# Kernel tuning notes

Hardware: AMD Instinct MI355X
Metric: run time of the kernel (lower is better)

## Reference

```python
import jax, jax.numpy as jnp
import numpy as np

D_MODEL = 1024
HEADDIM = 64
EXPAND = 2
D_STATE = 128
D_CONV = 4
NGROUPS = 1
D_INNER = EXPAND * D_MODEL            # 2048
NHEADS = D_INNER // HEADDIM           # 32
CONV_DIM = D_INNER + 2 * NGROUPS * D_STATE
D_IN_PROJ = 2 * D_INNER + 2 * NGROUPS * D_STATE + NHEADS
BATCH = 2
SEQLEN = 1024
EPS = 1e-5


def silu(v):
    return v * jax.nn.sigmoid(v)


def setup_inputs() -> dict:
    key = jax.random.key(0)
    ks = jax.random.split(key, 8)
    s = 0.02
    return {
        "x": jax.random.normal(ks[0], (BATCH, SEQLEN, D_MODEL), jnp.float32),
        "in_proj_w": jax.random.normal(ks[1], (D_IN_PROJ, D_MODEL), jnp.float32) * s,
        "conv_w": jax.random.normal(ks[2], (CONV_DIM, D_CONV), jnp.float32) * 0.2,
        "conv_b": jax.random.normal(ks[3], (CONV_DIM,), jnp.float32) * 0.02,
        "dt_bias": jax.random.normal(ks[4], (NHEADS,), jnp.float32) * 0.1,
        "A_log": jax.random.normal(ks[5], (NHEADS,), jnp.float32) * 0.5,
        "D": jax.random.normal(ks[6], (NHEADS,), jnp.float32) * 0.5,
        "norm_w": jnp.ones((D_INNER,), jnp.float32),
        "out_proj_w": jax.random.normal(ks[7], (D_MODEL, D_INNER), jnp.float32) * s,
    }


def _mamba2(x, in_proj_w, conv_w, conv_b, dt_bias, A_log, D, norm_w, out_proj_w):
    b, l, _ = x.shape
    # input projection -> z | xBC | dt
    zxbcdt = x @ in_proj_w.T                                  # [b,l,d_in_proj]
    z, xBC, dt = jnp.split(zxbcdt, [D_INNER, D_INNER + CONV_DIM], axis=-1)
    dt = jax.nn.softplus(dt + dt_bias)                        # [b,l,nh]
    # causal depthwise conv over time, then SiLU
    rhs = conv_w.T[:, None, :]                                # [d_conv, 1, conv_dim]
    xBC = jax.lax.conv_general_dilated(
        xBC, rhs, window_strides=(1,), padding=[(D_CONV - 1, 0)],
        dimension_numbers=("NWC", "WIO", "NWC"), feature_group_count=CONV_DIM)
    xBC = silu(xBC + conv_b)
    xs, Bm, Cm = jnp.split(xBC, [D_INNER, D_INNER + D_STATE], axis=-1)
    xs = xs.reshape(b, l, NHEADS, HEADDIM)                    # [b,l,h,p]
    A = -jnp.exp(A_log)                                       # [nh], negative
    dA = jnp.exp(dt * A)                                      # [b,l,nh] in (0,1)
    # selective scan: h_t = dA_t * h_{t-1} + dt_t * x_t (outer) B_t; y_t = h_t C_t
    def step(h, inp):
        dA_t, x_t, B_t, dt_t, C_t = inp                       # [b,h],[b,h,p],[b,n],[b,h],[b,n]
        h = h * dA_t[:, :, None, None] + jnp.einsum("bh,bhp,bn->bhpn", dt_t, x_t, B_t)
        y = jnp.einsum("bhpn,bn->bhp", h, C_t)
        return h, y

    h0 = jnp.zeros((b, NHEADS, HEADDIM, D_STATE), x.dtype)
    xs_t = xs.transpose(1, 0, 2, 3)
    _, ys = jax.lax.scan(step, h0, (dA.transpose(1, 0, 2), xs_t,
                                    Bm.transpose(1, 0, 2), dt.transpose(1, 0, 2),
                                    Cm.transpose(1, 0, 2)))
    y = ys.transpose(1, 0, 2, 3) + D[None, None, :, None] * xs  # skip term
    y = y.reshape(b, l, D_INNER)
    # gated RMSNorm (norm_before_gate=False): rmsnorm(y * silu(z)) * w
    y = y * silu(z)
    y = y * jax.lax.rsqrt(jnp.mean(y * y, axis=-1, keepdims=True) + EPS) * norm_w
    return y @ out_proj_w.T


def reference(x, in_proj_w, conv_w, conv_b, dt_bias, A_log, D, norm_w, out_proj_w):
    return x + _mamba2(x, in_proj_w, conv_w, conv_b, dt_bias, A_log, D, norm_w, out_proj_w)
```

## Files before the change

### kernel.cpp

```cpp
#include <hip/hip_runtime.h>
#include <hip/hip_bf16.h>
#include <math.h>

#define NHEADS   32
#define CONV_DIM 2304
#define D_INNER  2048
#define SEQLEN   1024
#define NROWS    2048
#define ZX_STR   4352
#define D_MODEL  1024
#define Q        64
#define NCHUNK   16
#define XT_STR   72

typedef __attribute__((ext_vector_type(8))) short bhalf8;
typedef __attribute__((ext_vector_type(8))) short short8;
typedef __attribute__((ext_vector_type(4))) short short4v;
typedef __attribute__((ext_vector_type(4))) float f32x4;

__device__ __forceinline__ float bf2f(__hip_bfloat16 v){ return __bfloat162float(v); }
__device__ __forceinline__ short f2bs(float f){ __hip_bfloat16 h = __float2bfloat16(f); return *(short*)&h; }
__device__ __forceinline__ float s2f(short s){ __hip_bfloat16 h = *(__hip_bfloat16*)&s; return __bfloat162float(h); }
__device__ __forceinline__ float rdin(const void* p, size_t i, int isf){
    return isf ? ((const float*)p)[i] : __bfloat162float(((const __hip_bfloat16*)p)[i]);
}

__global__ __launch_bounds__(256)
void detect_dtype(const unsigned short* __restrict__ p, int* __restrict__ flag)
{
    int cnt = 0;
    for (int i = threadIdx.x; i < 4096; i += 256) {
        unsigned short u = p[2 * i];
        int e = (u >> 7) & 0xFF;
        cnt += (e >= 90 && e <= 141) ? 1 : 0;
    }
#pragma unroll
    for (int m = 1; m < 64; m <<= 1) cnt += __shfl_xor(cnt, m);
    __shared__ int red[4];
    if ((threadIdx.x & 63) == 0) red[threadIdx.x >> 6] = cnt;
    __syncthreads();
    if (threadIdx.x == 0) *flag = ((red[0]+red[1]+red[2]+red[3]) < 2048) ? 1 : 0;
}

#define XN8 262144
#define WN8 561152
#define ON8 262144
__global__ __launch_bounds__(256)
void to_bf16_all(const void* __restrict__ xs, const void* __restrict__ ws,
                 const void* __restrict__ os,
                 __hip_bfloat16* __restrict__ xd, __hip_bfloat16* __restrict__ wd,
                 __hip_bfloat16* __restrict__ od, const int* __restrict__ flagp)
{
    const int isf = *flagp;
    int i = blockIdx.x * 256 + threadIdx.x;
    const void* src; __hip_bfloat16* dst; int j;
    if (i < XN8)            { src = xs; dst = xd; j = i; }
    else if (i < XN8 + WN8) { src = ws; dst = wd; j = i - XN8; }
    else                    { src = os; dst = od; j = i - XN8 - WN8; }
    if (isf) {
        const float4* s = (const float4*)src;
        float4 a = s[2 * j], b = s[2 * j + 1];
        short8 r;
        r[0]=f2bs(a.x); r[1]=f2bs(a.y); r[2]=f2bs(a.z); r[3]=f2bs(a.w);
        r[4]=f2bs(b.x); r[5]=f2bs(b.y); r[6]=f2bs(b.z); r[7]=f2bs(b.w);
        ((short8*)dst)[j] = r;
    } else {
        ((float4*)dst)[j] = ((const float4*)src)[j];
    }
}

template<int MODE, int MT, int NT, int WROWS, int WCOLS>
__global__ __launch_bounds__(256)
void gemm_bt(const __hip_bfloat16* __restrict__ A,
             const __hip_bfloat16* __restrict__ W,
             __hip_bfloat16* __restrict__ Cb,
             const void* __restrict__ xraw,
             void* __restrict__ outv,
             const int* __restrict__ flagp,
             int K, int N)
{
    constexpr int FM = MT / WROWS / 16;
    constexpr int FN = NT / WCOLS / 16;
    constexpr int AI = MT / 32;
    constexpr int BI = NT / 32;
    __shared__ short As[MT * 64];
    __shared__ short Bs[NT * 64];
    const int m0 = blockIdx.y * MT;
    const int n0 = blockIdx.x * NT;
    const int wave = threadIdx.x >> 6;
    const int lane = threadIdx.x & 63;
    const int lr8 = lane >> 3, lc8 = lane & 7;
    const int lr  = lane & 15, lq  = lane >> 4;
    const int wm = (wave / WCOLS) * (MT / WROWS);
    const int wn = (wave % WCOLS) * (NT / WCOLS);
    const int swl = lr & 7;

    f32x4 acc[FM][FN];
#pragma unroll
    for (int i = 0; i < FM; ++i)
#pragma unroll
        for (int j = 0; j < FN; ++j) acc[i][j] = (f32x4){0.f,0.f,0.f,0.f};

    for (int k0 = 0; k0 < K; k0 += 64) {
#pragma unroll
        for (int i = 0; i < AI; ++i) {
            const int rt = (wave * AI + i) * 8;
            const __hip_bfloat16* gp = A + (size_t)(m0 + rt + lr8) * K + k0 + ((lc8 ^ lr8) << 3);
            __builtin_amdgcn_global_load_lds(
                (const __attribute__((address_space(1))) void*)gp,
                (__attribute__((address_space(3))) void*)&As[rt * 64], 16, 0, 0);
        }
#pragma unroll
        for (int i = 0; i < BI; ++i) {
            const int rt = (wave * BI + i) * 8;
            const __hip_bfloat16* gp = W + (size_t)(n0 + rt + lr8) * K + k0 + ((lc8 ^ lr8) << 3);
            __builtin_amdgcn_global_load_lds(
                (const __attribute__((address_space(1))) void*)gp,
                (__attribute__((address_space(3))) void*)&Bs[rt * 64], 16, 0, 0);
        }
        __syncthreads();
#pragma unroll
        for (int kk = 0; kk < 64; kk += 32) {
            const int sw = (((kk >> 3) + lq) ^ swl) << 3;
            bhalf8 af[FM], bfv[FN];
#pragma unroll
            for (int t = 0; t < FM; ++t)
                af[t]  = *(const bhalf8*)&As[(wm + t * 16 + lr) * 64 + sw];
#pragma unroll
            for (int t = 0; t < FN; ++t)
                bfv[t] = *(const bhalf8*)&Bs[(wn + t * 16 + lr) * 64 + sw];
#pragma unroll
            for (int ti = 0; ti < FM; ++ti)
#pragma unroll
                for (int tj = 0; tj < FN; ++tj)
                    acc[ti][tj] = __builtin_amdgcn_mfma_f32_16x16x32_bf16(
                        af[ti], bfv[tj], acc[ti][tj], 0, 0, 0);
        }
        __syncthreads();
    }

    const int isf = (MODE == 1) ? *flagp : 0;
#pragma unroll
    for (int ti = 0; ti < FM; ++ti)
#pragma unroll
        for (int tj = 0; tj < FN; ++tj)
#pragma unroll
            for (int r = 0; r < 4; ++r) {
                int m = m0 + wm + ti * 16 + lq * 4 + r;
                int n = n0 + wn + tj * 16 + lr;
                size_t idx = (size_t)m * N + n;
                float v = acc[ti][tj][r];
                if (MODE == 0) {
                    Cb[idx] = __float2bfloat16(v);
                } else {
                    v += rdin(xraw, idx, isf);
                    if (isf) ((float*)outv)[idx] = v;
                    else     ((__hip_bfloat16*)outv)[idx] = __float2bfloat16(v);
                }
            }
}

__global__ __launch_bounds__(256)
void dt_kernel(const void* __restrict__ xraw, const void* __restrict__ wraw,
               const void* __restrict__ dt_bias,
               const int* __restrict__ flagp,
               float* __restrict__ dtp)
{
    const int isf = *flagp;
    const int r0 = blockIdx.x * 8;
    __shared__ float xs[8][D_MODEL];
    for (int idx = threadIdx.x; idx < 8 * D_MODEL; idx += 256)
        ((float*)xs)[idx] = rdin(xraw, (size_t)r0 * D_MODEL + idx, isf);
    __syncthreads();
    const int h = threadIdx.x >> 3;
    const int t = threadIdx.x & 7;
    const size_t wbase = (size_t)(4352 + h) * D_MODEL;
    float s[8];
#pragma unroll
    for (int r = 0; r < 8; ++r) s[r] = 0.f;
    for (int k = t; k < D_MODEL; k += 8) {
        float wv = rdin(wraw, wbase + k, isf);
#pragma unroll
        for (int r = 0; r < 8; ++r) s[r] = fmaf(xs[r][k], wv, s[r]);
    }
#pragma unroll
    for (int r = 0; r < 8; ++r) {
        s[r] += __shfl_xor(s[r], 1);
        s[r] += __shfl_xor(s[r], 2);
        s[r] += __shfl_xor(s[r], 4);
    }
    if (t == 0) {
        float bias = rdin(dt_bias, h, isf);
#pragma unroll
        for (int r = 0; r < 8; ++r) {
            float raw = s[r] + bias;
            dtp[(size_t)(r0 + r) * NHEADS + h] = raw > 20.f ? raw : log1pf(expf(raw));
        }
    }
}

__global__ __launch_bounds__(256)
void conv_silu(const __hip_bfloat16* __restrict__ zxb,
               const void* __restrict__ conv_w, const void* __restrict__ conv_b,
               const int* __restrict__ flagp,
               __hip_bfloat16* __restrict__ xs_bf,
               __hip_bfloat16* __restrict__ B_bf,
               __hip_bfloat16* __restrict__ C_bf)
{
    __shared__ short buf[11 * CONV_DIM];
    const int isf = *flagp;
    const int r0 = blockIdx.x * 8;
    const int bstart = r0 & ~(SEQLEN - 1);
    for (int idx = threadIdx.x; idx < 11 * (CONV_DIM / 8); idx += 256) {
        int ii = idx / (CONV_DIM / 8);
        int seg = idx % (CONV_DIM / 8);
        int g = r0 - 3 + ii;
        bhalf8 v;
        if (g >= bstart) {
            v = *(const bhalf8*)&zxb[(size_t)g * ZX_STR + 2048 + seg * 8];
        } else {
#pragma unroll
            for (int j = 0; j < 8; ++j) v[j] = 0;
        }
        *(bhalf8*)&buf[ii * CONV_DIM + seg * 8] = v;
    }
    __syncthreads();

#pragma unroll
    for (int j = 0; j < CONV_DIM / 256; ++j) {
        const int c = threadIdx.x + j * 256;
        float w0 = rdin(conv_w, (size_t)c * 4 + 0, isf);
        float w1 = rdin(conv_w, (size_t)c * 4 + 1, isf);
        float w2 = rdin(conv_w, (size_t)c * 4 + 2, isf);
        float w3 = rdin(conv_w, (size_t)c * 4 + 3, isf);
        float bias = rdin(conv_b, c, isf);
#pragma unroll
        for (int r = 0; r < 8; ++r) {
            float acc = bias;
            acc = fmaf(s2f(buf[(r + 0) * CONV_DIM + c]), w0, acc);
            acc = fmaf(s2f(buf[(r + 1) * CONV_DIM + c]), w1, acc);
            acc = fmaf(s2f(buf[(r + 2) * CONV_DIM + c]), w2, acc);
            acc = fmaf(s2f(buf[(r + 3) * CONV_DIM + c]), w3, acc);
            float v = acc / (1.f + expf(-acc));
            __hip_bfloat16 bv = __float2bfloat16(v);
            int row = r0 + r;
            if (c < 2048)       xs_bf[(size_t)row * 2048 + c] = bv;
            else if (c < 2176)  B_bf[(size_t)row * 128 + (c - 2048)] = bv;
            else                C_bf[(size_t)row * 128 + (c - 2176)] = bv;
        }
    }
}

__global__ __launch_bounds__(256)
void chunk_kernel(const __hip_bfloat16* __restrict__ xs_bf,
                  const __hip_bfloat16* __restrict__ B_bf,
                  const __hip_bfloat16* __restrict__ C_bf,
                  const float* __restrict__ dtp, const void* __restrict__ Alog,
                  const int* __restrict__ flagp,
                  float* __restrict__ cumg, float* __restrict__ decayg,
                  __hip_bfloat16* __restrict__ M_bf, float* __restrict__ S)
{
    __shared__ float cumS[Q], uS[Q], dtS[Q];
    __shared__ short Xt[64 * XT_STR];
    __shared__ short Bt[128 * XT_STR];
    const int bhc = blockIdx.x;
    const int c = bhc & 15, h = (bhc >> 4) & 31, b = bhc >> 9;
    const int row0 = b * SEQLEN + c * Q;
    const int isf = *flagp;

    if (threadIdx.x < 64) {
        const int t = threadIdx.x;
        const float An = -expf(rdin(Alog, h, isf));
        const float dt = dtp[(size_t)(row0 + t) * NHEADS + h];
        float cum = dt * An;
#pragma unroll
        for (int ofs = 1; ofs < 64; ofs <<= 1) {
            float v = __shfl_up(cum, ofs);
            if (t >= ofs) cum += v;
        }
        float tot = __shfl(cum, 63);
        cumS[t] = cum; dtS[t] = dt;
        uS[t] = expf(tot - cum) * dt;
        cumg[(size_t)bhc * Q + t] = cum;
        if (t == 63) decayg[bhc] = expf(tot);
    }
    __syncthreads();

#pragma unroll
    for (int i = 0; i < 2; ++i) {
        int seg = threadIdx.x + i * 256;
        int t = seg >> 3, p8 = (seg & 7) * 8;
        float ut = uS[t];
        bhalf8 v = *(const bhalf8*)&xs_bf[(size_t)(row0 + t) * 2048 + h * 64 + p8];
#pragma unroll
        for (int j = 0; j < 8; ++j)
            Xt[(p8 + j) * XT_STR + t] = f2bs(s2f(v[j]) * ut);
    }
#pragma unroll
    for (int i = 0; i < 4; ++i) {
        int seg = threadIdx.x + i * 256;
        int t = seg >> 4, n8 = (seg & 15) * 8;
        bhalf8 v = *(const bhalf8*)&B_bf[(size_t)(row0 + t) * 128 + n8];
#pragma unroll
        for (int j = 0; j < 8; ++j)
            Bt[(n8 + j) * XT_STR + t] = v[j];
    }

    const int wave = threadIdx.x >> 6, lane = threadIdx.x & 63;
    const int lr = lane & 15, lq = lane >> 4;

    {
        const int t0 = wave * 16;
        f32x4 acc[4];
#pragma unroll
        for (int j = 0; j < 4; ++j) acc[j] = (f32x4){0.f,0.f,0.f,0.f};
#pragma unroll
        for (int kk = 0; kk < 128; kk += 32) {
            bhalf8 af = *(const bhalf8*)&C_bf[(size_t)(row0 + t0 + lr) * 128 + kk + lq * 8];
#pragma unroll
            for (int j = 0; j < 4; ++j) {
                bhalf8 bf = *(const bhalf8*)&B_bf[(size_t)(row0 + j * 16 + lr) * 128 + kk + lq * 8];
                acc[j] = __builtin_amdgcn_mfma_f32_16x16x32_bf16(af, bf, acc[j], 0, 0, 0);
            }
        }
#pragma unroll
        for (int j = 0; j < 4; ++j)
#pragma unroll
            for (int r = 0; r < 4; ++r) {
                int t = t0 + lq * 4 + r;
                int s = j * 16 + lr;
                float m = (s <= t) ? acc[j][r] * expf(cumS[t] - cumS[s]) * dtS[s] : 0.f;
                M_bf[(size_t)bhc * 4096 + t * 64 + s] = __float2bfloat16(m);
            }
    }
    __syncthreads();

    {
        const int p0 = wave * 16;
        f32x4 acc[8];
#pragma unroll
        for (int j = 0; j < 8; ++j) acc[j] = (f32x4){0.f,0.f,0.f,0.f};
#pragma unroll
        for (int kk = 0; kk < 64; kk += 32) {
            bhalf8 af = *(const bhalf8*)&Xt[(p0 + lr) * XT_STR + kk + lq * 8];
#pragma unroll
            for (int j = 0; j < 8; ++j) {
                bhalf8 bf = *(const bhalf8*)&Bt[(j * 16 + lr) * XT_STR + kk + lq * 8];
                acc[j] = __builtin_amdgcn_mfma_f32_16x16x32_bf16(af, bf, acc[j], 0, 0, 0);
            }
        }
#pragma unroll
        for (int j = 0; j < 8; ++j)
#pragma unroll
            for (int r = 0; r < 4; ++r) {
                int p = p0 + lq * 4 + r;
                int n = j * 16 + lr;
                S[(size_t)bhc * 8192 + p * 128 + n] = acc[j][r];
            }
    }
}

__global__ __launch_bounds__(256)
void rec_kernel(const float* __restrict__ S, const float* __restrict__ decayg,
                __hip_bfloat16* __restrict__ hst)
{
    const int bh = blockIdx.x >> 3;
    const int sl = blockIdx.x & 7;
    const int off = sl * 1024 + threadIdx.x * 4;
    float h0 = 0.f, h1 = 0.f, h2 = 0.f, h3 = 0.f;
    for (int c = 0; c < NCHUNK; ++c) {
        size_t base = ((size_t)bh * NCHUNK + c) * 8192 + off;
        short4v hb;
        hb[0] = f2bs(h0); hb[1] = f2bs(h1); hb[2] = f2bs(h2); hb[3] = f2bs(h3);
        *(short4v*)&hst[base] = hb;
        float4 s = *(const float4*)&S[base];
        float d = decayg[bh * NCHUNK + c];
        h0 = fmaf(h0, d, s.x); h1 = fmaf(h1, d, s.y);
        h2 = fmaf(h2, d, s.z); h3 = fmaf(h3, d, s.w);
    }
}

__global__ __launch_bounds__(256)
void y_kernel(const __hip_bfloat16* __restrict__ M_bf,
              const __hip_bfloat16* __restrict__ xs_bf,
              const __hip_bfloat16* __restrict__ C_bf,
              const __hip_bfloat16* __restrict__ hst,
              const float* __restrict__ cumg,
              const void* __restrict__ Draw, const int* __restrict__ flagp,
              float* __restrict__ yws)
{
    __shared__ short Xt[64 * XT_STR];
    const int bhc = blockIdx.x;
    const int c = bhc & 15, h = (bhc >> 4) & 31, b = bhc >> 9;
    const int row0 = b * SEQLEN + c * Q;
    const int isf = *flagp;
    const float Dh = rdin(Draw, h, isf);

#pragma unroll
    for (int i = 0; i < 2; ++i) {
        int seg = threadIdx.x + i * 256;
        int t = seg >> 3, p8 = (seg & 7) * 8;
        bhalf8 v = *(const bhalf8*)&xs_bf[(size_t)(row0 + t) * 2048 + h * 64 + p8];
#pragma unroll
        for (int j = 0; j < 8; ++j)
            Xt[(p8 + j) * XT_STR + t] = v[j];
    }
    __syncthreads();

    const int wave = threadIdx.x >> 6, lane = threadIdx.x & 63;
    const int lr = lane & 15, lq = lane >> 4;
    const int t0 = wave * 16;
    f32x4 acc1[4], acc2[4];
#pragma unroll
    for (int j = 0; j < 4; ++j) { acc1[j] = (f32x4){0.f,0.f,0.f,0.f}; acc2[j] = acc1[j]; }

#pragma unroll
    for (int kk = 0; kk < 64; kk += 32) {
        bhalf8 af = *(const bhalf8*)&M_bf[(size_t)bhc * 4096 + (t0 + lr) * 64 + kk + lq * 8];
#pragma unroll
        for (int j = 0; j < 4; ++j) {
            bhalf8 bf = *(const bhalf8*)&Xt[(j * 16 + lr) * XT_STR + kk + lq * 8];
            acc1[j] = __builtin_amdgcn_mfma_f32_16x16x32_bf16(af, bf, acc1[j], 0, 0, 0);
        }
    }
#pragma unroll
    for (int kk = 0; kk < 128; kk += 32) {
        bhalf8 af = *(const bhalf8*)&C_bf[(size_t)(row0 + t0 + lr) * 128 + kk + lq * 8];
#pragma unroll
        for (int j = 0; j < 4; ++j) {
            bhalf8 bf = *(const bhalf8*)&hst[(size_t)bhc * 8192 + (j * 16 + lr) * 128 + kk + lq * 8];
            acc2[j] = __builtin_amdgcn_mfma_f32_16x16x32_bf16(af, bf, acc2[j], 0, 0, 0);
        }
    }
    float ex[4];
#pragma unroll
    for (int r = 0; r < 4; ++r) ex[r] = expf(cumg[(size_t)bhc * Q + t0 + lq * 4 + r]);
#pragma unroll
    for (int j = 0; j < 4; ++j)
#pragma unroll
        for (int r = 0; r < 4; ++r) {
            int t = t0 + lq * 4 + r;
            int p = j * 16 + lr;
            float xv = s2f(Xt[p * XT_STR + t]);
            float y = acc1[j][r] + ex[r] * acc2[j][r] + Dh * xv;
            yws[(size_t)(row0 + t) * D_INNER + h * 64 + p] = y;
        }
}

__global__ __launch_bounds__(256)
void gate_norm(const float* __restrict__ yws,
               const __hip_bfloat16* __restrict__ zxb,
               const void* __restrict__ norm_w,
               const int* __restrict__ flagp,
               __hip_bfloat16* __restrict__ yg)
{
    const int isf = *flagp;
    const int row = blockIdx.x;
    const float* y = yws + (size_t)row * D_INNER;
    const __hip_bfloat16* z = zxb + (size_t)row * ZX_STR;
    float v[8]; float ss = 0.f;
#pragma unroll
    for (int it = 0; it < 8; ++it) {
        int c = it * 256 + threadIdx.x;
        float zz = bf2f(z[c]);
        float vv = y[c] * (zz / (1.f + expf(-zz)));
        v[it] = vv;
        ss += vv * vv;
    }
#pragma unroll
    for (int m = 1; m < 64; m <<= 1) ss += __shfl_xor(ss, m);
    __shared__ float red[4];
    if ((threadIdx.x & 63) == 0) red[threadIdx.x >> 6] = ss;
    __syncthreads();
    float tot = red[0] + red[1] + red[2] + red[3];
    float scale = rsqrtf(tot / (float)D_INNER + 1e-5f);
#pragma unroll
    for (int it = 0; it < 8; ++it) {
        int c = it * 256 + threadIdx.x;
        yg[(size_t)row * D_INNER + c] =
            __float2bfloat16(v[it] * scale * rdin(norm_w, c, isf));
    }
}

extern "C" void kernel_launch(void* const* d_in, const int* in_sizes, int n_in,
                              void* d_out, int out_size, void* d_ws, size_t ws_size,
                              hipStream_t stream)
{
    const void* x_raw    = d_in[0];
    const void* inw_raw  = d_in[1];
    const void* convw    = d_in[2];
    const void* convb    = d_in[3];
    const void* dtb      = d_in[4];
    const void* Alog     = d_in[5];
    const void* Dsk      = d_in[6];
    const void* normw    = d_in[7];
    const void* outw_raw = d_in[8];

    char* ws = (char*)d_ws;
    size_t off = 0;
    int* flag = (int*)(ws + off);                      off += 256;
    __hip_bfloat16* xb    = (__hip_bfloat16*)(ws+off); off += (size_t)NROWS * D_MODEL * 2;
    __hip_bfloat16* inwb  = (__hip_bfloat16*)(ws+off); off += (size_t)4384 * D_MODEL * 2;
    __hip_bfloat16* outwb = (__hip_bfloat16*)(ws+off); off += (size_t)D_MODEL * D_INNER * 2;
    __hip_bfloat16* zxb   = (__hip_bfloat16*)(ws+off); off += (size_t)NROWS * ZX_STR * 2;
    __hip_bfloat16* xs_bf = (__hip_bfloat16*)(ws+off); off += (size_t)NROWS * 2048 * 2;
    __hip_bfloat16* B_bf  = (__hip_bfloat16*)(ws+off); off += (size_t)NROWS * 128 * 2;
    __hip_bfloat16* C_bf  = (__hip_bfloat16*)(ws+off); off += (size_t)NROWS * 128 * 2;
    float* dtp   = (float*)(ws+off);                   off += (size_t)NROWS * NHEADS * 4;
    float* cumg  = (float*)(ws+off);                   off += (size_t)1024 * Q * 4;
    float* decayg= (float*)(ws+off);                   off += (size_t)1024 * 4;
    __hip_bfloat16* M_bf  = (__hip_bfloat16*)(ws+off); off += (size_t)1024 * 4096 * 2;
    __hip_bfloat16* hst   = (__hip_bfloat16*)(ws+off); off += (size_t)1024 * 8192 * 2;
    float* S = (float*)(ws+off);                       off += (size_t)1024 * 8192 * 4;
    float* yws = S;
    __hip_bfloat16* yg = (__hip_bfloat16*)(S + (size_t)NROWS * D_INNER);

    detect_dtype<<<1, 256, 0, stream>>>((const unsigned short*)x_raw, flag);
    to_bf16_all<<<(XN8+WN8+ON8)/256, 256, 0, stream>>>(x_raw, inw_raw, outw_raw,
                                                       xb, inwb, outwb, flag);
    gemm_bt<0,64,128,1,4><<<dim3(34, 32), 256, 0, stream>>>(
        xb, inwb, zxb, nullptr, nullptr, flag, D_MODEL, ZX_STR);
    dt_kernel<<<256, 256, 0, stream>>>(x_raw, inw_raw, dtb, flag, dtp);
    conv_silu<<<256, 256, 0, stream>>>(zxb, convw, convb, flag, xs_bf, B_bf, C_bf);
    chunk_kernel<<<1024, 256, 0, stream>>>(xs_bf, B_bf, C_bf, dtp, Alog, flag,
                                           cumg, decayg, M_bf, S);
    rec_kernel<<<512, 256, 0, stream>>>(S, decayg, hst);
    y_kernel<<<1024, 256, 0, stream>>>(M_bf, xs_bf, C_bf, hst, cumg, Dsk, flag, yws);
    gate_norm<<<NROWS, 256, 0, stream>>>(yws, zxb, normw, flag, yg);
    gemm_bt<1,64,64,2,2><<<dim3(16, 32), 256, 0, stream>>>(
        yg, outwb, nullptr, x_raw, d_out, flag, D_INNER, D_MODEL);
}
```

Baseline: 256.7 us.

## Fuse conv/dt kernels, gate into y_kernel, and store chunk states in bf16

Merges the dt projection and causal conv kernels into one launch split by block index, and vectorizes the conv to 8-channel bf16 loads and stores. Moves the SiLU gating and the sum of squares into y_kernel, using atomics into a per-row accumulator that detect_dtype zeroes, so the final pass only applies the RMS scale. It also stores chunk states and the gated output in bf16 instead of fp32 to halve that traffic. The cost is extra rounding in the state recurrence and the pre-norm values, plus atomic contention on row sums.

Result: faster. 248.8 us (-3.1%).

```diff
diff --git a/kernel.cpp b/kernel.cpp
--- a/kernel.cpp
+++ b/kernel.cpp
@@ -26,8 +26,10 @@
 }
 
 __global__ __launch_bounds__(256)
-void detect_dtype(const unsigned short* __restrict__ p, int* __restrict__ flag)
-{
+void detect_dtype(const unsigned short* __restrict__ p, int* __restrict__ flag,
+                  float* __restrict__ rowsum)
+{
+    for (int i = threadIdx.x; i < NROWS; i += 256) rowsum[i] = 0.f;
     int cnt = 0;
     for (int i = threadIdx.x; i < 4096; i += 256) {
         unsigned short u = p[2 * i];
@@ -161,92 +163,106 @@
 }
 
 __global__ __launch_bounds__(256)
-void dt_kernel(const void* __restrict__ xraw, const void* __restrict__ wraw,
-               const void* __restrict__ dt_bias,
-               const int* __restrict__ flagp,
-               float* __restrict__ dtp)
-{
+void convdt(const __hip_bfloat16* __restrict__ zxb,
+            const void* __restrict__ conv_w, const void* __restrict__ conv_b,
+            const void* __restrict__ xraw, const void* __restrict__ wraw,
+            const void* __restrict__ dt_bias,
+            const int* __restrict__ flagp,
+            __hip_bfloat16* __restrict__ xs_bf,
+            __hip_bfloat16* __restrict__ B_bf,
+            __hip_bfloat16* __restrict__ C_bf,
+            float* __restrict__ dtp)
+{
+    __shared__ short smem[11 * CONV_DIM];
     const int isf = *flagp;
-    const int r0 = blockIdx.x * 8;
-    __shared__ float xs[8][D_MODEL];
-    for (int idx = threadIdx.x; idx < 8 * D_MODEL; idx += 256)
-        ((float*)xs)[idx] = rdin(xraw, (size_t)r0 * D_MODEL + idx, isf);
-    __syncthreads();
-    const int h = threadIdx.x >> 3;
-    const int t = threadIdx.x & 7;
-    const size_t wbase = (size_t)(4352 + h) * D_MODEL;
-    float s[8];
-#pragma unroll
-    for (int r = 0; r < 8; ++r) s[r] = 0.f;
-    for (int k = t; k < D_MODEL; k += 8) {
-        float wv = rdin(wraw, wbase + k, isf);
-#pragma unroll
-        for (int r = 0; r < 8; ++r) s[r] = fmaf(xs[r][k], wv, s[r]);
-    }
-#pragma unroll
-    for (int r = 0; r < 8; ++r) {
-        s[r] += __shfl_xor(s[r], 1);
-        s[r] += __shfl_xor(s[r], 2);
-        s[r] += __shfl_xor(s[r], 4);
-    }
-    if (t == 0) {
-        float bias = rdin(dt_bias, h, isf);
+
+    if (blockIdx.x < 256) {
+        const int r0 = blockIdx.x * 8;
+        const int bstart = r0 & ~(SEQLEN - 1);
+        for (int idx = threadIdx.x; idx < 11 * (CONV_DIM / 8); idx += 256) {
+            int ii = idx / (CONV_DIM / 8);
+            int seg = idx % (CONV_DIM / 8);
+            int g = r0 - 3 + ii;
+            bhalf8 v;
+            if (g >= bstart) {
+                v = *(const bhalf8*)&zxb[(size_t)g * ZX_STR + 2048 + seg * 8];
+            } else {
+#pragma unroll
+                for (int j = 0; j < 8; ++j) v[j] = 0;
+            }
+            *(bhalf8*)&smem[ii * CONV_DIM + seg * 8] = v;
+        }
+        __syncthreads();
+
+#pragma unroll
+        for (int sIt = 0; sIt < 2; ++sIt) {
+            const int seg = threadIdx.x + sIt * 256;
+            if (seg >= CONV_DIM / 8) break;
+            const int c0 = seg * 8;
+            float w0[8], w1[8], w2[8], w3[8], bias[8];
+#pragma unroll
+            for (int j = 0; j < 8; ++j) {
+                bias[j] = rdin(conv_b, c0 + j, isf);
+                w0[j] = rdin(conv_w, (size_t)(c0 + j) * 4 + 0, isf);
+                w1[j] = rdin(conv_w, (size_t)(c0 + j) * 4 + 1, isf);
+                w2[j] = rdin(conv_w, (size_t)(c0 + j) * 4 + 2, isf);
+                w3[j] = rdin(conv_w, (size_t)(c0 + j) * 4 + 3, isf);
+            }
+#pragma unroll
+            for (int r = 0; r < 8; ++r) {
+                bhalf8 i0 = *(const bhalf8*)&smem[(r + 0) * CONV_DIM + c0];
+                bhalf8 i1 = *(const bhalf8*)&smem[(r + 1) * CONV_DIM + c0];
+                bhalf8 i2 = *(const bhalf8*)&smem[(r + 2) * CONV_DIM + c0];
+                bhalf8 i3 = *(const bhalf8*)&smem[(r + 3) * CONV_DIM + c0];
+                bhalf8 out;
+#pragma unroll
+                for (int j = 0; j < 8; ++j) {
+                    float acc = bias[j];
+                    acc = fmaf(s2f(i0[j]), w0[j], acc);
+                    acc = fmaf(s2f(i1[j]), w1[j], acc);
+                    acc = fmaf(s2f(i2[j]), w2[j], acc);
+                    acc = fmaf(s2f(i3[j]), w3[j], acc);
+                    out[j] = f2bs(acc / (1.f + expf(-acc)));
+                }
+                const int row = r0 + r;
+                if (c0 < 2048)
+                    *(bhalf8*)&xs_bf[(size_t)row * 2048 + c0] = out;
+                else if (c0 < 2176)
+                    *(bhalf8*)&B_bf[(size_t)row * 128 + (c0 - 2048)] = out;
+                else
+                    *(bhalf8*)&C_bf[(size_t)row * 128 + (c0 - 2176)] = out;
+            }
+        }
+    } else {
+        float* xsh = (float*)smem;
+        const int r0 = (blockIdx.x - 256) * 8;
+        for (int idx = threadIdx.x; idx < 8 * D_MODEL; idx += 256)
+            xsh[idx] = rdin(xraw, (size_t)r0 * D_MODEL + idx, isf);
+        __syncthreads();
+        const int h = threadIdx.x >> 3;
+        const int t = threadIdx.x & 7;
+        const size_t wbase = (size_t)(4352 + h) * D_MODEL;
+        float s[8];
+#pragma unroll
+        for (int r = 0; r < 8; ++r) s[r] = 0.f;
+        for (int k = t; k < D_MODEL; k += 8) {
+            float wv = rdin(wraw, wbase + k, isf);
+#pragma unroll
+            for (int r = 0; r < 8; ++r) s[r] = fmaf(xsh[r * D_MODEL + k], wv, s[r]);
+        }
 #pragma unroll
         for (int r = 0; r < 8; ++r) {
-            float raw = s[r] + bias;
-            dtp[(size_t)(r0 + r) * NHEADS + h] = raw > 20.f ? raw : log1pf(expf(raw));
-        }
-    }
-}
-
-__global__ __launch_bounds__(256)
-void conv_silu(const __hip_bfloat16* __restrict__ zxb,
-               const void* __restrict__ conv_w, const void* __restrict__ conv_b,
-               const int* __restrict__ flagp,
-               __hip_bfloat16* __restrict__ xs_bf,
-               __hip_bfloat16* __restrict__ B_bf,
-               __hip_bfloat16* __restrict__ C_bf)
-{
-    __shared__ short buf[11 * CONV_DIM];
-    const int isf = *flagp;
-    const int r0 = blockIdx.x * 8;
-    const int bstart = r0 & ~(SEQLEN - 1);
-    for (int idx = threadIdx.x; idx < 11 * (CONV_DIM / 8); idx += 256) {
-        int ii = idx / (CONV_DIM / 8);
-        int seg = idx % (CONV_DIM / 8);
-        int g = r0 - 3 + ii;
-        bhalf8 v;
-        if (g >= bstart) {
-            v = *(const bhalf8*)&zxb[(size_t)g * ZX_STR + 2048 + seg * 8];
-        } else {
-#pragma unroll
-            for (int j = 0; j < 8; ++j) v[j] = 0;
-        }
-        *(bhalf8*)&buf[ii * CONV_DIM + seg * 8] = v;
-    }
-    __syncthreads();
-
-#pragma unroll
-    for (int j = 0; j < CONV_DIM / 256; ++j) {
-        const int c = threadIdx.x + j * 256;
-        float w0 = rdin(conv_w, (size_t)c * 4 + 0, isf);
-        float w1 = rdin(conv_w, (size_t)c * 4 + 1, isf);
-        float w2 = rdin(conv_w, (size_t)c * 4 + 2, isf);
-        float w3 = rdin(conv_w, (size_t)c * 4 + 3, isf);
-        float bias = rdin(conv_b, c, isf);
-#pragma unroll
-        for (int r = 0; r < 8; ++r) {
-            float acc = bias;
-            acc = fmaf(s2f(buf[(r + 0) * CONV_DIM + c]), w0, acc);
-            acc = fmaf(s2f(buf[(r + 1) * CONV_DIM + c]), w1, acc);
-            acc = fmaf(s2f(buf[(r + 2) * CONV_DIM + c]), w2, acc);
-            acc = fmaf(s2f(buf[(r + 3) * CONV_DIM + c]), w3, acc);
-            float v = acc / (1.f + expf(-acc));
-            __hip_bfloat16 bv = __float2bfloat16(v);
-            int row = r0 + r;
-            if (c < 2048)       xs_bf[(size_t)row * 2048 + c] = bv;
-            else if (c < 2176)  B_bf[(size_t)row * 128 + (c - 2048)] = bv;
-            else                C_bf[(size_t)row * 128 + (c - 2176)] = bv;
+            s[r] += __shfl_xor(s[r], 1);
+            s[r] += __shfl_xor(s[r], 2);
+            s[r] += __shfl_xor(s[r], 4);
+        }
+        if (t == 0) {
+            float bias = rdin(dt_bias, h, isf);
+#pragma unroll
+            for (int r = 0; r < 8; ++r) {
+                float raw = s[r] + bias;
+                dtp[(size_t)(r0 + r) * NHEADS + h] = raw > 20.f ? raw : log1pf(expf(raw));
+            }
         }
     }
 }
@@ -258,7 +274,8 @@
                   const float* __restrict__ dtp, const void* __restrict__ Alog,
                   const int* __restrict__ flagp,
                   float* __restrict__ cumg, float* __restrict__ decayg,
-                  __hip_bfloat16* __restrict__ M_bf, float* __restrict__ S)
+                  __hip_bfloat16* __restrict__ M_bf,
+                  __hip_bfloat16* __restrict__ Sb)
 {
     __shared__ float cumS[Q], uS[Q], dtS[Q];
     __shared__ short Xt[64 * XT_STR];
@@ -355,13 +372,14 @@
             for (int r = 0; r < 4; ++r) {
                 int p = p0 + lq * 4 + r;
                 int n = j * 16 + lr;
-                S[(size_t)bhc * 8192 + p * 128 + n] = acc[j][r];
-            }
-    }
-}
-
-__global__ __launch_bounds__(256)
-void rec_kernel(const float* __restrict__ S, const float* __restrict__ decayg,
+                Sb[(size_t)bhc * 8192 + p * 128 + n] = __float2bfloat16(acc[j][r]);
+            }
+    }
+}
+
+__global__ __launch_bounds__(256)
+void rec_kernel(const __hip_bfloat16* __restrict__ Sb,
+                const float* __restrict__ decayg,
                 __hip_bfloat16* __restrict__ hst)
 {
     const int bh = blockIdx.x >> 3;
@@ -373,10 +391,10 @@
         short4v hb;
         hb[0] = f2bs(h0); hb[1] = f2bs(h1); hb[2] = f2bs(h2); hb[3] = f2bs(h3);
         *(short4v*)&hst[base] = hb;
-        float4 s = *(const float4*)&S[base];
+        short4v sv = *(const short4v*)&Sb[base];
         float d = decayg[bh * NCHUNK + c];
-        h0 = fmaf(h0, d, s.x); h1 = fmaf(h1, d, s.y);
-        h2 = fmaf(h2, d, s.z); h3 = fmaf(h3, d, s.w);
+        h0 = fmaf(h0, d, s2f(sv[0])); h1 = fmaf(h1, d, s2f(sv[1]));
+        h2 = fmaf(h2, d, s2f(sv[2])); h3 = fmaf(h3, d, s2f(sv[3]));
     }
 }
 
@@ -386,10 +404,12 @@
               const __hip_bfloat16* __restrict__ C_bf,
               const __hip_bfloat16* __restrict__ hst,
               const float* __restrict__ cumg,
+              const __hip_bfloat16* __restrict__ zxb,
               const void* __restrict__ Draw, const int* __restrict__ flagp,
-              float* __restrict__ yws)
+              __hip_bfloat16* __restrict__ vbuf, float* __restrict__ rowsum)
 {
     __shared__ short Xt[64 * XT_STR];
+    __shared__ short zS[64 * XT_STR];
     const int bhc = blockIdx.x;
     const int c = bhc & 15, h = (bhc >> 4) & 31, b = bhc >> 9;
     const int row0 = b * SEQLEN + c * Q;
@@ -404,6 +424,8 @@
 #pragma unroll
         for (int j = 0; j < 8; ++j)
             Xt[(p8 + j) * XT_STR + t] = v[j];
+        bhalf8 zv = *(const bhalf8*)&zxb[(size_t)(row0 + t) * ZX_STR + h * 64 + p8];
+        *(bhalf8*)&zS[t * XT_STR + p8] = zv;
     }
     __syncthreads();
 
@@ -435,6 +457,9 @@
     float ex[4];
 #pragma unroll
     for (int r = 0; r < 4; ++r) ex[r] = expf(cumg[(size_t)bhc * Q + t0 + lq * 4 + r]);
+
+    float vv[4][4];
+    float s2[4] = {0.f, 0.f, 0.f, 0.f};
 #pragma unroll
     for (int j = 0; j < 4; ++j)
 #pragma unroll
@@ -443,43 +468,56 @@
             int p = j * 16 + lr;
             float xv = s2f(Xt[p * XT_STR + t]);
             float y = acc1[j][r] + ex[r] * acc2[j][r] + Dh * xv;
-            yws[(size_t)(row0 + t) * D_INNER + h * 64 + p] = y;
-        }
-}
-
-__global__ __launch_bounds__(256)
-void gate_norm(const float* __restrict__ yws,
-               const __hip_bfloat16* __restrict__ zxb,
-               const void* __restrict__ norm_w,
-               const int* __restrict__ flagp,
-               __hip_bfloat16* __restrict__ yg)
+            float zz = s2f(zS[t * XT_STR + p]);
+            float v = y * (zz / (1.f + expf(-zz)));
+            vv[j][r] = v;
+            s2[r] += v * v;
+        }
+#pragma unroll
+    for (int r = 0; r < 4; ++r) {
+        s2[r] += __shfl_xor(s2[r], 1);
+        s2[r] += __shfl_xor(s2[r], 2);
+        s2[r] += __shfl_xor(s2[r], 4);
+        s2[r] += __shfl_xor(s2[r], 8);
+    }
+    if (lr == 0)
+#pragma unroll
+        for (int r = 0; r < 4; ++r)
+            atomicAdd(&rowsum[row0 + t0 + lq * 4 + r], s2[r]);
+
+    __syncthreads();
+#pragma unroll
+    for (int j = 0; j < 4; ++j)
+#pragma unroll
+        for (int r = 0; r < 4; ++r)
+            zS[(t0 + lq * 4 + r) * XT_STR + j * 16 + lr] = f2bs(vv[j][r]);
+    __syncthreads();
+#pragma unroll
+    for (int i = 0; i < 2; ++i) {
+        int seg = threadIdx.x + i * 256;
+        int t = seg >> 3, p8 = (seg & 7) * 8;
+        bhalf8 o = *(const bhalf8*)&zS[t * XT_STR + p8];
+        *(bhalf8*)&vbuf[(size_t)(row0 + t) * D_INNER + h * 64 + p8] = o;
+    }
+}
+
+__global__ __launch_bounds__(256)
+void gate_scale(const __hip_bfloat16* __restrict__ vbuf,
+                const float* __restrict__ rowsum,
+                const void* __restrict__ norm_w,
+                const int* __restrict__ flagp,
+                __hip_bfloat16* __restrict__ yg)
 {
     const int isf = *flagp;
     const int row = blockIdx.x;
-    const float* y = yws + (size_t)row * D_INNER;
-    const __hip_bfloat16* z = zxb + (size_t)row * ZX_STR;
-    float v[8]; float ss = 0.f;
-#pragma unroll
-    for (int it = 0; it < 8; ++it) {
-        int c = it * 256 + threadIdx.x;
-        float zz = bf2f(z[c]);
-        float vv = y[c] * (zz / (1.f + expf(-zz)));
-        v[it] = vv;
-        ss += vv * vv;
-    }
-#pragma unroll
-    for (int m = 1; m < 64; m <<= 1) ss += __shfl_xor(ss, m);
-    __shared__ float red[4];
-    if ((threadIdx.x & 63) == 0) red[threadIdx.x >> 6] = ss;
-    __syncthreads();
-    float tot = red[0] + red[1] + red[2] + red[3];
-    float scale = rsqrtf(tot / (float)D_INNER + 1e-5f);
-#pragma unroll
-    for (int it = 0; it < 8; ++it) {
-        int c = it * 256 + threadIdx.x;
-        yg[(size_t)row * D_INNER + c] =
-            __float2bfloat16(v[it] * scale * rdin(norm_w, c, isf));
-    }
+    const float scale = rsqrtf(rowsum[row] / (float)D_INNER + 1e-5f);
+    const int seg = threadIdx.x;
+    bhalf8 v8 = *(const bhalf8*)&vbuf[(size_t)row * D_INNER + seg * 8];
+    bhalf8 o;
+#pragma unroll
+    for (int j = 0; j < 8; ++j)
+        o[j] = f2bs(s2f(v8[j]) * scale * rdin(norm_w, seg * 8 + j, isf));
+    *(bhalf8*)&yg[(size_t)row * D_INNER + seg * 8] = o;
 }
 
 extern "C" void kernel_launch(void* const* d_in, const int* in_sizes, int n_in,
@@ -499,6 +537,7 @@
     char* ws = (char*)d_ws;
     size_t off = 0;
     int* flag = (int*)(ws + off);                      off += 256;
+    float* rowsum = (float*)(ws + off);                off += (size_t)NROWS * 4;
     __hip_bfloat16* xb    = (__hip_bfloat16*)(ws+off); off += (size_t)NROWS * D_MODEL * 2;
     __hip_bfloat16* inwb  = (__hip_bfloat16*)(ws+off); off += (size_t)4384 * D_MODEL * 2;
     __hip_bfloat16* outwb = (__hip_bfloat16*)(ws+off); off += (size_t)D_MODEL * D_INNER * 2;
@@ -511,22 +550,23 @@
     float* decayg= (float*)(ws+off);                   off += (size_t)1024 * 4;
     __hip_bfloat16* M_bf  = (__hip_bfloat16*)(ws+off); off += (size_t)1024 * 4096 * 2;
     __hip_bfloat16* hst   = (__hip_bfloat16*)(ws+off); off += (size_t)1024 * 8192 * 2;
-    float* S = (float*)(ws+off);                       off += (size_t)1024 * 8192 * 4;
-    float* yws = S;
-    __hip_bfloat16* yg = (__hip_bfloat16*)(S + (size_t)NROWS * D_INNER);
-
-    detect_dtype<<<1, 256, 0, stream>>>((const unsigned short*)x_raw, flag);
+    __hip_bfloat16* Sb    = (__hip_bfloat16*)(ws+off); off += (size_t)1024 * 8192 * 2;
+    __hip_bfloat16* vbuf = Sb;
+    __hip_bfloat16* yg   = Sb + (size_t)NROWS * D_INNER;
+
+    detect_dtype<<<1, 256, 0, stream>>>((const unsigned short*)x_raw, flag, rowsum);
     to_bf16_all<<<(XN8+WN8+ON8)/256, 256, 0, stream>>>(x_raw, inw_raw, outw_raw,
                                                        xb, inwb, outwb, flag);
     gemm_bt<0,64,128,1,4><<<dim3(34, 32), 256, 0, stream>>>(
         xb, inwb, zxb, nullptr, nullptr, flag, D_MODEL, ZX_STR);
-    dt_kernel<<<256, 256, 0, stream>>>(x_raw, inw_raw, dtb, flag, dtp);
-    conv_silu<<<256, 256, 0, stream>>>(zxb, convw, convb, flag, xs_bf, B_bf, C_bf);
+    convdt<<<512, 256, 0, stream>>>(zxb, convw, convb, x_raw, inw_raw, dtb, flag,
+                                    xs_bf, B_bf, C_bf, dtp);
     chunk_kernel<<<1024, 256, 0, stream>>>(xs_bf, B_bf, C_bf, dtp, Alog, flag,
-                                           cumg, decayg, M_bf, S);
-    rec_kernel<<<512, 256, 0, stream>>>(S, decayg, hst);
-    y_kernel<<<1024, 256, 0, stream>>>(M_bf, xs_bf, C_bf, hst, cumg, Dsk, flag, yws);
-    gate_norm<<<NROWS, 256, 0, stream>>>(yws, zxb, normw, flag, yg);
+                                           cumg, decayg, M_bf, Sb);
+    rec_kernel<<<512, 256, 0, stream>>>(Sb, decayg, hst);
+    y_kernel<<<1024, 256, 0, stream>>>(M_bf, xs_bf, C_bf, hst, cumg, zxb, Dsk,
+                                       flag, vbuf, rowsum);
+    gate_scale<<<NROWS, 256, 0, stream>>>(vbuf, rowsum, normw, flag, yg);
     gemm_bt<1,64,64,2,2><<<dim3(16, 32), 256, 0, stream>>>(
         yg, outwb, nullptr, x_raw, d_out, flag, D_INNER, D_MODEL);
 }
```
